# Performance work log

Hardware: AMD Instinct MI355X
Metric: run time of the kernel (lower is better)

The kernel has to match this reference:

```python
import jax, jax.numpy as jnp
import numpy as np

B, I, H = 8192, 1024, 1024

def _xavier(key, out_f, in_f):
    limit = (6.0 / (in_f + out_f)) ** 0.5
    return jax.random.uniform(key, (out_f, in_f), jnp.float32, -limit, limit)

def setup_inputs() -> dict:
    key = jax.random.key(0)
    ks = jax.random.split(key, 11)
    inp = {
        'x': jax.random.normal(ks[0], (B, I), jnp.float32),
        'h': jax.random.normal(ks[1], (B, H), jnp.float32),
        'c': jax.random.normal(ks[2], (B, H), jnp.float32),
    }
    names = ['Wxi', 'Whi', 'Wxf', 'Whf', 'Wxo', 'Who', 'Wxg', 'Whg']
    for n, k in zip(names, ks[3:]):
        in_f = I if n[1] == 'x' else H
        inp[n + '_w'] = _xavier(k, H, in_f)
        inp[n + '_b'] = jnp.zeros((H,), jnp.float32)
    return inp

def reference(x, h, c,
              Wxi_w, Wxi_b, Whi_w, Whi_b,
              Wxf_w, Wxf_b, Whf_w, Whf_b,
              Wxo_w, Wxo_b, Who_w, Who_b,
              Wxg_w, Wxg_b, Whg_w, Whg_b):
    Wx = jnp.concatenate([Wxi_w, Wxf_w, Wxo_w, Wxg_w], axis=0)  # [4H, I]
    Wh = jnp.concatenate([Whi_w, Whf_w, Who_w, Whg_w], axis=0)  # [4H, H]
    bx = jnp.concatenate([Wxi_b, Wxf_b, Wxo_b, Wxg_b], axis=0)  # [4H]
    bh = jnp.concatenate([Whi_b, Whf_b, Who_b, Whg_b], axis=0)  # [4H]
    z = x @ Wx.T + bx + h @ Wh.T + bh  # [B, 4H]
    zi, zf, zo, zg = jnp.split(z, 4, axis=-1)
    it = jax.nn.sigmoid(zi)
    ft = jax.nn.sigmoid(zf)
    ot = jax.nn.sigmoid(zo)
    gt = jnp.tanh(zg)
    c_next = ft * c + it * gt
    h_next = ot * jnp.tanh(c_next)
    return (h_next, c_next)
```

## Files before the change

### kernel.cpp

```cpp
#include <hip/hip_runtime.h>
#include <hip/hip_bf16.h>
#include <cstdint>


typedef __bf16 bf16;
typedef __attribute__((ext_vector_type(8))) bf16 bf16x8;
typedef __attribute__((ext_vector_type(4))) float f32x4;

#define CN_OFF 8388608

__device__ __forceinline__ void gload16(const bf16* g, bf16* l) {
  __builtin_amdgcn_global_load_lds(
      (const __attribute__((address_space(1))) void*)g,
      (__attribute__((address_space(3))) void*)l, 16, 0, 0);
}

__device__ __forceinline__ bf16x8 cvt8(f32x4 v0, f32x4 v1) {
  bf16x8 o;
  o[0]=(bf16)v0[0]; o[1]=(bf16)v0[1]; o[2]=(bf16)v0[2]; o[3]=(bf16)v0[3];
  o[4]=(bf16)v1[0]; o[5]=(bf16)v1[1]; o[6]=(bf16)v1[2]; o[7]=(bf16)v1[3];
  return o;
}

__global__ __launch_bounds__(256) void pack_all(
    const float* __restrict__ x, const float* __restrict__ h,
    const float* __restrict__ wxi, const float* __restrict__ whi,
    const float* __restrict__ wxf, const float* __restrict__ whf,
    const float* __restrict__ wxo, const float* __restrict__ who,
    const float* __restrict__ wxg, const float* __restrict__ whg,
    const float* __restrict__ bxi, const float* __restrict__ bhi,
    const float* __restrict__ bxf, const float* __restrict__ bhf,
    const float* __restrict__ bxo, const float* __restrict__ bho,
    const float* __restrict__ bxg, const float* __restrict__ bhg,
    bf16* __restrict__ A2, bf16* __restrict__ B2, float* __restrict__ Bcomb) {
  __shared__ __align__(16) bf16 lds[8192];
  const int t = threadIdx.x;
  const int bid = blockIdx.x;

  if (bid < 2048) {
    const int mb = bid >> 5;
    const int wm = (bid >> 4) & 1;
    const int q  = bid & 15;
    const int rowbase = mb * 128 + wm * 64;
    const float* srcM; int k0;
    if (q < 8) { srcM = x; k0 = q * 128; } else { srcM = h; k0 = q * 128 - 1024; }
#pragma unroll
    for (int r = 0; r < 4; ++r) {
      const int rl = r * 16 + (t >> 4);
      const int cc = (t & 15) * 8;
      const float* s = srcM + (size_t)(rowbase + rl) * 1024 + k0 + cc;
      f32x4 v0 = *(const f32x4*)s;
      f32x4 v1 = *(const f32x4*)(s + 4);
      const int chunkS = (t & 15) ^ (rl & 7);
      *(bf16x8*)((char*)lds + rl * 256 + chunkS * 16) = cvt8(v0, v1);
    }
    __syncthreads();
#pragma unroll
    for (int r = 0; r < 4; ++r) {
      const int idx = r * 256 + t;
      const int fj  = idx >> 6;
      const int ktL = fj >> 2, mi = fj & 3;
      const int l   = idx & 63;
      const int srow = mi * 16 + (l & 15);
      const int chunkS = (ktL * 4 + (l >> 4)) ^ (srow & 7);
      bf16x8 o = *(const bf16x8*)((const char*)lds + srow * 256 + chunkS * 16);
      size_t el = ((size_t)mb * 64 + q * 4 + ktL) * 4096 + (size_t)wm * 2048 + mi * 512 + l * 8;
      *(bf16x8*)(A2 + el) = o;
    }
  } else {
    const int bid2 = bid - 2048;
    const int nb   = bid2 >> 6;
    const int gate = (bid2 >> 4) & 3;
    const int q    = bid2 & 15;
    const float* wxm = (gate == 0) ? wxi : (gate == 1) ? wxf : (gate == 2) ? wxo : wxg;
    const float* whm = (gate == 0) ? whi : (gate == 1) ? whf : (gate == 2) ? who : whg;
    const float* srcM; int k0;
    if (q < 8) { srcM = wxm; k0 = q * 128; } else { srcM = whm; k0 = q * 128 - 1024; }
    const int jbase = nb * 32;
#pragma unroll
    for (int r = 0; r < 2; ++r) {
      const int rl = r * 16 + (t >> 4);
      const int cc = (t & 15) * 8;
      const float* s = srcM + (size_t)(jbase + rl) * 1024 + k0 + cc;
      f32x4 v0 = *(const f32x4*)s;
      f32x4 v1 = *(const f32x4*)(s + 4);
      const int chunkS = (t & 15) ^ (rl & 7);
      *(bf16x8*)((char*)lds + rl * 256 + chunkS * 16) = cvt8(v0, v1);
    }
    __syncthreads();
#pragma unroll
    for (int r = 0; r < 2; ++r) {
      const int idx = r * 256 + t;
      const int fj  = idx >> 6;
      const int ktL = fj >> 1, wn = fj & 1;
      const int l   = idx & 63;
      const int srow = wn * 16 + (l & 15);
      const int chunkS = (ktL * 4 + (l >> 4)) ^ (srow & 7);
      bf16x8 o = *(const bf16x8*)((const char*)lds + srow * 256 + chunkS * 16);
      size_t el = ((size_t)nb * 64 + q * 4 + ktL) * 4096 + (size_t)wn * 2048 + gate * 512 + l * 8;
      *(bf16x8*)(B2 + el) = o;
    }
    if (q == 0 && t < 32) {
      const float* bxv = (gate == 0) ? bxi : (gate == 1) ? bxf : (gate == 2) ? bxo : bxg;
      const float* bhv = (gate == 0) ? bhi : (gate == 1) ? bhf : (gate == 2) ? bho : bhg;
      const int wn = t >> 4, jl = t & 15;
      const int j = nb * 32 + wn * 16 + jl;
      Bcomb[(nb * 2 + wn) * 64 + gate * 16 + jl] = bxv[j] + bhv[j];
    }
  }
}

__device__ __forceinline__ float sigf(float v) { return 1.f / (1.f + __expf(-v)); }
__device__ __forceinline__ float tanhfast(float v) {
  v = fminf(15.f, fmaxf(-15.f, v));
  float e = __expf(2.f * v);
  return (e - 1.f) / (e + 1.f);
}

__global__ __launch_bounds__(512, 2) void gemm_lstm(const bf16* __restrict__ A2,
                                                    const bf16* __restrict__ B2,
                                                    const float* __restrict__ Bcomb,
                                                    const float* __restrict__ c,
                                                    float* __restrict__ out) {
  __shared__ __align__(16) bf16 lds[65536];
  const int t    = threadIdx.x;
  const int wave = t >> 6;
  const int lane = t & 63;

  const int bid = blockIdx.x;
  const int xcd = bid & 7;
  const int idx = bid >> 3;
  const int bn  = xcd * 2 + (idx & 1);
  const int bm  = idx >> 1;

  const int wr  = wave >> 2;
  const int wc  = wave & 3;
  const int nbL = wc >> 1, wn = wc & 1;
  const int lrow = lane & 15, lkg = lane >> 4;

  const int tEl = t * 8;
  const int wEl = (t & ~63) * 8;

  const bf16* aSrc0 = A2 + (size_t)(2 * bm)     * 64 * 4096;
  const bf16* aSrc1 = A2 + (size_t)(2 * bm + 1) * 64 * 4096;
  const bf16* bSrc0 = B2 + (size_t)(2 * bn)     * 64 * 4096;
  const bf16* bSrc1 = B2 + (size_t)(2 * bn + 1) * 64 * 4096;

  auto stage = [&](int tile, int buf) {
    const size_t kOff = (size_t)tile * 4096;
    bf16* d = lds + buf * 16384;
    gload16(aSrc0 + kOff + tEl, d +         wEl);
    gload16(aSrc1 + kOff + tEl, d +  4096 + wEl);
    gload16(bSrc0 + kOff + tEl, d +  8192 + wEl);
    gload16(bSrc1 + kOff + tEl, d + 12288 + wEl);
  };

  f32x4 acc[8][4] = {};

  stage(0, 0);
  stage(1, 1);

  for (int kt = 0; kt < 64; ++kt) {
    const int p = kt & 3;
    if (kt < 63) asm volatile("s_waitcnt vmcnt(4)" ::: "memory");
    else         asm volatile("s_waitcnt vmcnt(0)" ::: "memory");
    __builtin_amdgcn_s_barrier();
    asm volatile("" ::: "memory");
    if (kt + 2 < 64) stage(kt + 2, (kt + 2) & 3);

    const bf16* bufA = lds + p * 16384 + wr * 4096;
    const bf16* bufB = lds + p * 16384 + 8192 + nbL * 4096 + wn * 2048;
    bf16x8 af[8], bfr[4];
#pragma unroll
    for (int i = 0; i < 8; ++i)
      af[i] = *(const bf16x8*)(bufA + i * 512 + lane * 8);
#pragma unroll
    for (int g = 0; g < 4; ++g)
      bfr[g] = *(const bf16x8*)(bufB + g * 512 + lane * 8);
    __builtin_amdgcn_s_setprio(1);
#pragma unroll
    for (int i = 0; i < 8; ++i)
#pragma unroll
      for (int g = 0; g < 4; ++g)
        acc[i][g] = __builtin_amdgcn_mfma_f32_16x16x32_bf16(af[i], bfr[g], acc[i][g], 0, 0, 0);
    __builtin_amdgcn_s_setprio(0);
  }

  const int nb = bn * 2 + nbL;
  const int jg = (nb * 2 + wn) * 16 + lrow;
  const int bbase = (nb * 2 + wn) * 64 + lrow;
  const float bi  = Bcomb[bbase +  0];
  const float bf_ = Bcomb[bbase + 16];
  const float bo  = Bcomb[bbase + 32];
  const float bg  = Bcomb[bbase + 48];

#pragma unroll
  for (int i = 0; i < 8; ++i) {
    const int row0 = (2 * bm + wr) * 128 + (i >> 2) * 64 + (i & 3) * 16 + lkg * 4;
    float cv[4];
#pragma unroll
    for (int r = 0; r < 4; ++r)
      cv[r] = c[(size_t)(row0 + r) * 1024 + jg];
#pragma unroll
    for (int r = 0; r < 4; ++r) {
      float zi = acc[i][0][r] + bi;
      float zf = acc[i][1][r] + bf_;
      float zo = acc[i][2][r] + bo;
      float zg = acc[i][3][r] + bg;
      float it = sigf(zi), ft = sigf(zf), ot = sigf(zo), gt = tanhfast(zg);
      float cn = ft * cv[r] + it * gt;
      size_t off = (size_t)(row0 + r) * 1024 + jg;
      out[off] = ot * tanhfast(cn);
      out[CN_OFF + off] = cn;
    }
  }
}

extern "C" void kernel_launch(void* const* d_in, const int* in_sizes, int n_in,
                              void* d_out, int out_size, void* d_ws, size_t ws_size,
                              hipStream_t stream) {
  const float* x   = (const float*)d_in[0];
  const float* h   = (const float*)d_in[1];
  const float* c   = (const float*)d_in[2];
  const float* Wxi = (const float*)d_in[3];  const float* bxi = (const float*)d_in[4];
  const float* Whi = (const float*)d_in[5];  const float* bhi = (const float*)d_in[6];
  const float* Wxf = (const float*)d_in[7];  const float* bxf = (const float*)d_in[8];
  const float* Whf = (const float*)d_in[9];  const float* bhf = (const float*)d_in[10];
  const float* Wxo = (const float*)d_in[11]; const float* bxo = (const float*)d_in[12];
  const float* Who = (const float*)d_in[13]; const float* bho = (const float*)d_in[14];
  const float* Wxg = (const float*)d_in[15]; const float* bxg = (const float*)d_in[16];
  const float* Whg = (const float*)d_in[17]; const float* bhg = (const float*)d_in[18];
  float* out = (float*)d_out;

  bf16*  Abuf  = (bf16*)d_ws;
  bf16*  Wbuf  = Abuf + (size_t)8192 * 2048;
  float* Bcomb = (float*)(Wbuf + (size_t)4096 * 2048);

  pack_all<<<4096, 256, 0, stream>>>(x, h,
                                     Wxi, Whi, Wxf, Whf, Wxo, Who, Wxg, Whg,
                                     bxi, bhi, bxf, bhf, bxo, bho, bxg, bhg,
                                     Abuf, Wbuf, Bcomb);
  gemm_lstm<<<512, 512, 0, stream>>>(Abuf, Wbuf, Bcomb, c, out);
}
```

Before: 319.1 us.

## Deepen LDS prefetch to three tiles and split each K-step into two phases

The K-loop pipeline goes from prefetching two tiles ahead to three ahead, using all four LDS buffers. Each iteration is split into two halves, with A-fragment loads, a half-tile global->LDS stage, and MFMAs interleaved between extra barriers. The aim is to hide global load latency and spread the memory issue across the compute phase. In exchange it adds more barriers per iteration, turns off loop unrolling, and needs careful vmcnt accounting that could race if miscounted.

```diff
diff --git a/kernel.cpp b/kernel.cpp
--- a/kernel.cpp
+++ b/kernel.cpp
@@ -146,44 +146,67 @@
   const bf16* bSrc0 = B2 + (size_t)(2 * bn)     * 64 * 4096;
   const bf16* bSrc1 = B2 + (size_t)(2 * bn + 1) * 64 * 4096;
 
-  auto stage = [&](int tile, int buf) {
+  auto stageHalf = [&](int tile, int half) {
     const size_t kOff = (size_t)tile * 4096;
-    bf16* d = lds + buf * 16384;
-    gload16(aSrc0 + kOff + tEl, d +         wEl);
-    gload16(aSrc1 + kOff + tEl, d +  4096 + wEl);
-    gload16(bSrc0 + kOff + tEl, d +  8192 + wEl);
-    gload16(bSrc1 + kOff + tEl, d + 12288 + wEl);
+    bf16* d = lds + (tile & 3) * 16384;
+    if (half == 0) {
+      gload16(aSrc0 + kOff + tEl, d +        wEl);
+      gload16(aSrc1 + kOff + tEl, d + 4096 + wEl);
+    } else {
+      gload16(bSrc0 + kOff + tEl, d +  8192 + wEl);
+      gload16(bSrc1 + kOff + tEl, d + 12288 + wEl);
+    }
   };
 
   f32x4 acc[8][4] = {};
 
-  stage(0, 0);
-  stage(1, 1);
-
+  stageHalf(0, 0); stageHalf(0, 1);
+  stageHalf(1, 0); stageHalf(1, 1);
+  stageHalf(2, 0); stageHalf(2, 1);
+  asm volatile("s_waitcnt vmcnt(8)" ::: "memory");
+  __builtin_amdgcn_s_barrier();
+
+#pragma unroll 1
   for (int kt = 0; kt < 64; ++kt) {
     const int p = kt & 3;
-    if (kt < 63) asm volatile("s_waitcnt vmcnt(4)" ::: "memory");
-    else         asm volatile("s_waitcnt vmcnt(0)" ::: "memory");
-    __builtin_amdgcn_s_barrier();
-    asm volatile("" ::: "memory");
-    if (kt + 2 < 64) stage(kt + 2, (kt + 2) & 3);
-
     const bf16* bufA = lds + p * 16384 + wr * 4096;
     const bf16* bufB = lds + p * 16384 + 8192 + nbL * 4096 + wn * 2048;
     bf16x8 af[8], bfr[4];
-#pragma unroll
-    for (int i = 0; i < 8; ++i)
+
+#pragma unroll
+    for (int i = 0; i < 4; ++i)
       af[i] = *(const bf16x8*)(bufA + i * 512 + lane * 8);
 #pragma unroll
     for (int g = 0; g < 4; ++g)
       bfr[g] = *(const bf16x8*)(bufB + g * 512 + lane * 8);
+    if (kt <= 60) stageHalf(kt + 3, 0);
+    __builtin_amdgcn_s_barrier();
     __builtin_amdgcn_s_setprio(1);
 #pragma unroll
-    for (int i = 0; i < 8; ++i)
+    for (int i = 0; i < 4; ++i)
 #pragma unroll
       for (int g = 0; g < 4; ++g)
         acc[i][g] = __builtin_amdgcn_mfma_f32_16x16x32_bf16(af[i], bfr[g], acc[i][g], 0, 0, 0);
     __builtin_amdgcn_s_setprio(0);
+    __builtin_amdgcn_s_barrier();
+
+#pragma unroll
+    for (int i = 4; i < 8; ++i)
+      af[i] = *(const bf16x8*)(bufA + i * 512 + lane * 8);
+    if (kt <= 60) stageHalf(kt + 3, 1);
+    __builtin_amdgcn_s_barrier();
+    __builtin_amdgcn_s_setprio(1);
+#pragma unroll
+    for (int i = 4; i < 8; ++i)
+#pragma unroll
+      for (int g = 0; g < 4; ++g)
+        acc[i][g] = __builtin_amdgcn_mfma_f32_16x16x32_bf16(af[i], bfr[g], acc[i][g], 0, 0, 0);
+    __builtin_amdgcn_s_setprio(0);
+
+    if (kt <= 60)      asm volatile("s_waitcnt vmcnt(8)" ::: "memory");
+    else if (kt == 61) asm volatile("s_waitcnt vmcnt(4)" ::: "memory");
+    else if (kt == 62) asm volatile("s_waitcnt vmcnt(0)" ::: "memory");
+    if (kt < 63) __builtin_amdgcn_s_barrier();
   }
 
   const int nb = bn * 2 + nbL;
```

Result: slower. 328.6 us (+3.0%).

## Halve GEMM block N-tile, triple-buffer LDS, and raise occupancy to four blocks per CU

Applied to the files above, without the earlier changes.

Each GEMM block now covers 256x128 of the output instead of 256x256. Its accumulator array drops from 8x4 to 4x4, and shared memory goes from four 32KB stages to three 24KB stages. The grid doubles to 1024 blocks and launch bounds ask for four blocks per CU, to hide latency with more resident waves. The k-loop is unrolled by three so the buffer indices are compile-time constants. The cost is lower arithmetic intensity: each A tile is loaded twice as often from L2/HBM, and the pipeline is shallower.

```diff
diff --git a/kernel.cpp b/kernel.cpp
--- a/kernel.cpp
+++ b/kernel.cpp
@@ -117,12 +117,12 @@
   return (e - 1.f) / (e + 1.f);
 }
 
-__global__ __launch_bounds__(512, 2) void gemm_lstm(const bf16* __restrict__ A2,
+__global__ __launch_bounds__(512, 4) void gemm_lstm(const bf16* __restrict__ A2,
                                                     const bf16* __restrict__ B2,
                                                     const float* __restrict__ Bcomb,
                                                     const float* __restrict__ c,
                                                     float* __restrict__ out) {
-  __shared__ __align__(16) bf16 lds[65536];
+  __shared__ __align__(16) bf16 lds[36864];
   const int t    = threadIdx.x;
   const int wave = t >> 6;
   const int lane = t & 63;
@@ -130,12 +130,12 @@
   const int bid = blockIdx.x;
   const int xcd = bid & 7;
   const int idx = bid >> 3;
-  const int bn  = xcd * 2 + (idx & 1);
-  const int bm  = idx >> 1;
-
-  const int wr  = wave >> 2;
-  const int wc  = wave & 3;
-  const int nbL = wc >> 1, wn = wc & 1;
+  const int nb  = xcd * 4 + (idx & 3);
+  const int bm  = idx >> 2;
+
+  const int wr  = wave >> 1;
+  const int wn  = wave & 1;
+  const int mbU = wr >> 1, wm = wr & 1;
   const int lrow = lane & 15, lkg = lane >> 4;
 
   const int tEl = t * 8;
@@ -143,50 +143,56 @@
 
   const bf16* aSrc0 = A2 + (size_t)(2 * bm)     * 64 * 4096;
   const bf16* aSrc1 = A2 + (size_t)(2 * bm + 1) * 64 * 4096;
-  const bf16* bSrc0 = B2 + (size_t)(2 * bn)     * 64 * 4096;
-  const bf16* bSrc1 = B2 + (size_t)(2 * bn + 1) * 64 * 4096;
+  const bf16* bSrc  = B2 + (size_t)nb           * 64 * 4096;
 
   auto stage = [&](int tile, int buf) {
     const size_t kOff = (size_t)tile * 4096;
-    bf16* d = lds + buf * 16384;
-    gload16(aSrc0 + kOff + tEl, d +         wEl);
-    gload16(aSrc1 + kOff + tEl, d +  4096 + wEl);
-    gload16(bSrc0 + kOff + tEl, d +  8192 + wEl);
-    gload16(bSrc1 + kOff + tEl, d + 12288 + wEl);
+    bf16* d = lds + buf * 12288;
+    gload16(aSrc0 + kOff + tEl, d +        wEl);
+    gload16(aSrc1 + kOff + tEl, d + 4096 + wEl);
+    gload16(bSrc  + kOff + tEl, d + 8192 + wEl);
   };
 
-  f32x4 acc[8][4] = {};
+  f32x4 acc[4][4] = {};
 
   stage(0, 0);
   stage(1, 1);
 
-  for (int kt = 0; kt < 64; ++kt) {
-    const int p = kt & 3;
-    if (kt < 63) asm volatile("s_waitcnt vmcnt(4)" ::: "memory");
-    else         asm volatile("s_waitcnt vmcnt(0)" ::: "memory");
+  const int aOff = mbU * 4096 + wm * 2048 + lane * 8;
+  const int bOff = 8192 + wn * 2048 + lane * 8;
+
+  auto body = [&](int kt, int p, int pn, bool doStage, bool last) {
+    if (last) asm volatile("s_waitcnt vmcnt(0)" ::: "memory");
+    else      asm volatile("s_waitcnt vmcnt(3)" ::: "memory");
     __builtin_amdgcn_s_barrier();
     asm volatile("" ::: "memory");
-    if (kt + 2 < 64) stage(kt + 2, (kt + 2) & 3);
-
-    const bf16* bufA = lds + p * 16384 + wr * 4096;
-    const bf16* bufB = lds + p * 16384 + 8192 + nbL * 4096 + wn * 2048;
-    bf16x8 af[8], bfr[4];
-#pragma unroll
-    for (int i = 0; i < 8; ++i)
-      af[i] = *(const bf16x8*)(bufA + i * 512 + lane * 8);
+    if (doStage) stage(kt + 2, pn);
+    const bf16* bufA = lds + p * 12288 + aOff;
+    const bf16* bufB = lds + p * 12288 + bOff;
+    bf16x8 af[4], bfr[4];
+#pragma unroll
+    for (int i = 0; i < 4; ++i)
+      af[i] = *(const bf16x8*)(bufA + i * 512);
 #pragma unroll
     for (int g = 0; g < 4; ++g)
-      bfr[g] = *(const bf16x8*)(bufB + g * 512 + lane * 8);
+      bfr[g] = *(const bf16x8*)(bufB + g * 512);
     __builtin_amdgcn_s_setprio(1);
 #pragma unroll
-    for (int i = 0; i < 8; ++i)
+    for (int mi = 0; mi < 4; ++mi)
 #pragma unroll
       for (int g = 0; g < 4; ++g)
-        acc[i][g] = __builtin_amdgcn_mfma_f32_16x16x32_bf16(af[i], bfr[g], acc[i][g], 0, 0, 0);
+        acc[mi][g] = __builtin_amdgcn_mfma_f32_16x16x32_bf16(af[mi], bfr[g], acc[mi][g], 0, 0, 0);
     __builtin_amdgcn_s_setprio(0);
+  };
+
+#pragma unroll 1
+  for (int base = 0; base < 63; base += 3) {
+    body(base,     0, 2, base     < 62, false);
+    body(base + 1, 1, 0, base + 1 < 62, false);
+    body(base + 2, 2, 1, base + 2 < 62, false);
   }
-
-  const int nb = bn * 2 + nbL;
+  body(63, 0, 0, false, true);
+
   const int jg = (nb * 2 + wn) * 16 + lrow;
   const int bbase = (nb * 2 + wn) * 64 + lrow;
   const float bi  = Bcomb[bbase +  0];
@@ -195,18 +201,18 @@
   const float bg  = Bcomb[bbase + 48];
 
 #pragma unroll
-  for (int i = 0; i < 8; ++i) {
-    const int row0 = (2 * bm + wr) * 128 + (i >> 2) * 64 + (i & 3) * 16 + lkg * 4;
+  for (int mi = 0; mi < 4; ++mi) {
+    const int row0 = bm * 256 + mbU * 128 + wm * 64 + mi * 16 + lkg * 4;
     float cv[4];
 #pragma unroll
     for (int r = 0; r < 4; ++r)
       cv[r] = c[(size_t)(row0 + r) * 1024 + jg];
 #pragma unroll
     for (int r = 0; r < 4; ++r) {
-      float zi = acc[i][0][r] + bi;
-      float zf = acc[i][1][r] + bf_;
-      float zo = acc[i][2][r] + bo;
-      float zg = acc[i][3][r] + bg;
+      float zi = acc[mi][0][r] + bi;
+      float zf = acc[mi][1][r] + bf_;
+      float zo = acc[mi][2][r] + bo;
+      float zg = acc[mi][3][r] + bg;
       float it = sigf(zi), ft = sigf(zf), ot = sigf(zo), gt = tanhfast(zg);
       float cn = ft * cv[r] + it * gt;
       size_t off = (size_t)(row0 + r) * 1024 + jg;
@@ -240,5 +246,5 @@
                                      Wxi, Whi, Wxf, Whf, Wxo, Who, Wxg, Whg,
                                      bxi, bhi, bxf, bhf, bxo, bho, bxg, bhg,
                                      Abuf, Wbuf, Bcomb);
-  gemm_lstm<<<512, 512, 0, stream>>>(Abuf, Wbuf, Bcomb, c, out);
-}
+  gemm_lstm<<<1024, 512, 0, stream>>>(Abuf, Wbuf, Bcomb, c, out);
+}
```

New measurement: 314.7 us. About the same (-1.4%).
